# Kernel optimization log

Hardware: AMD Instinct MI355X
Metric: run time of the kernel (lower is better)

The kernel has to match this reference:

```python
import jax, jax.numpy as jnp
import numpy as np

N = 50000      # nodes
E = 800000     # edges (before self loops)
IN = 128       # in_channels
C = 64         # out_channels per head
H = 4          # heads (both layers)
NEG_SLOPE = 0.2


def setup_inputs():
    key = jax.random.key(0)
    ks = jax.random.split(key, 14)
    nrm = lambda k, sh, s: jax.random.normal(k, sh, dtype=jnp.float32) * s
    x = nrm(ks[0], (N, IN), 1.0)
    edge_index = jax.random.randint(ks[1], (2, E), 0, N, dtype=jnp.int32)
    batch = jnp.zeros((N,), dtype=jnp.int32)
    edge_attr = jax.random.uniform(ks[2], (E, 1), dtype=jnp.float32)
    # layer 1 params (PyG GATConv: lin, att_src, att_dst, lin_edge, att_edge, bias)
    W1 = nrm(ks[3], (IN, H * C), 1.0 / np.sqrt(IN))
    We1 = nrm(ks[4], (1, H * C), 1.0)
    att_s1 = nrm(ks[5], (H, C), 1.0 / np.sqrt(C))
    att_d1 = nrm(ks[6], (H, C), 1.0 / np.sqrt(C))
    att_e1 = nrm(ks[7], (H, C), 1.0 / np.sqrt(C))
    b1 = jnp.zeros((H * C,), dtype=jnp.float32)
    # layer 2 params (in = H*C = 256)
    W2 = nrm(ks[8], (H * C, H * C), 1.0 / np.sqrt(H * C))
    We2 = nrm(ks[9], (1, H * C), 1.0)
    att_s2 = nrm(ks[10], (H, C), 1.0 / np.sqrt(C))
    att_d2 = nrm(ks[11], (H, C), 1.0 / np.sqrt(C))
    att_e2 = nrm(ks[12], (H, C), 1.0 / np.sqrt(C))
    b2 = jnp.zeros((H * C,), dtype=jnp.float32)
    return dict(x=x, edge_index=edge_index, batch=batch, edge_attr=edge_attr,
                W1=W1, We1=We1, att_s1=att_s1, att_d1=att_d1, att_e1=att_e1, b1=b1,
                W2=W2, We2=We2, att_s2=att_s2, att_d2=att_d2, att_e2=att_e2, b2=b2)


def gat_layer(h_in, src, dst, e_attr, W, We, att_s, att_d, att_e, b):
    n = h_in.shape[0]
    h = (h_in @ W).reshape(n, H, C)                      # [N,H,C]
    a_src = jnp.einsum('nhc,hc->nh', h, att_s)           # [N,H]
    a_dst = jnp.einsum('nhc,hc->nh', h, att_d)
    e = (e_attr @ We).reshape(-1, H, C)                  # [E',H,C]
    a_edge = jnp.einsum('ehc,hc->eh', e, att_e)          # [E',H]
    alpha = jax.nn.leaky_relu(a_src[src] + a_dst[dst] + a_edge, NEG_SLOPE)
    # softmax over edges grouped by destination node
    amax = jax.ops.segment_max(alpha, dst, num_segments=n)
    amax = jnp.where(jnp.isfinite(amax), amax, 0.0)
    ex = jnp.exp(alpha - amax[dst])
    denom = jax.ops.segment_sum(ex, dst, num_segments=n)
    a = ex / (denom[dst] + 1e-16)                        # [E',H]
    out = jax.ops.segment_sum(a[:, :, None] * h[src], dst, num_segments=n)
    return out.reshape(n, H * C) + b


def reference(x, edge_index, batch, edge_attr,
              W1, We1, att_s1, att_d1, att_e1, b1,
              W2, We2, att_s2, att_d2, att_e2, b2):
    n = x.shape[0]
    # PyG GATConv default: add self loops, self-loop edge_attr = mean fill
    loop = jnp.arange(n, dtype=edge_index.dtype)
    src = jnp.concatenate([edge_index[0], loop])
    dst = jnp.concatenate([edge_index[1], loop])
    ea_fill = jnp.broadcast_to(edge_attr.mean(axis=0, keepdims=True), (n, edge_attr.shape[1]))
    ea = jnp.concatenate([edge_attr, ea_fill], axis=0)
    h1 = gat_layer(x, src, dst, ea, W1, We1, att_s1, att_d1, att_e1, b1)
    h2 = gat_layer(h1, src, dst, ea, W2, We2, att_s2, att_d2, att_e2, b2)
    return h2
```

## Files before the change

### kernel.cpp

```cpp
#include <hip/hip_runtime.h>

#define NEG_SLOPE 0.2f

typedef __attribute__((ext_vector_type(8))) short bf16x8;
typedef __attribute__((ext_vector_type(4))) float f32x4;

__device__ inline unsigned short f2bf(float x) {
  unsigned int u = __float_as_uint(x);
  u += 0x7fffu + ((u >> 16) & 1u);
  return (unsigned short)(u >> 16);
}

__device__ inline unsigned fkey(float x) {
  unsigned u = __float_as_uint(x);
  return (u >> 31) ? ~u : (u | 0x80000000u);
}
__device__ inline float fkey_dec(unsigned k) {
  unsigned u = (k & 0x80000000u) ? (k ^ 0x80000000u) : ~k;
  return __uint_as_float(u);
}


__global__ void hist_kernel(const int* __restrict__ ei, int* __restrict__ counts,
                            int E, int Etot) {
  int e = blockIdx.x * blockDim.x + threadIdx.x;
  if (e >= Etot) return;
  int d = (e < E) ? ei[E + e] : (e - E);
  atomicAdd(&counts[d], 1);
}

__global__ void mean_kernel(const float* __restrict__ ea, float* __restrict__ part, int E) {
  int i = blockIdx.x * blockDim.x + threadIdx.x;
  float s = 0.f;
  for (; i < E; i += gridDim.x * blockDim.x) s += ea[i];
#pragma unroll
  for (int off = 1; off < 64; off <<= 1) s += __shfl_xor(s, off, 64);
  __shared__ float ws_[4];
  if ((threadIdx.x & 63) == 0) ws_[threadIdx.x >> 6] = s;
  __syncthreads();
  if (threadIdx.x == 0) part[blockIdx.x] = ws_[0] + ws_[1] + ws_[2] + ws_[3];
}

__global__ void scan_blocksum(const int* __restrict__ counts, int* __restrict__ bsum, int Nn) {
  int base = blockIdx.x * 4096 + threadIdx.x * 16;
  int s = 0;
#pragma unroll
  for (int i = 0; i < 16; i++) { int idx = base + i; if (idx < Nn) s += counts[idx]; }
#pragma unroll
  for (int off = 1; off < 64; off <<= 1) s += __shfl_xor(s, off, 64);
  __shared__ int ws_[4];
  if ((threadIdx.x & 63) == 0) ws_[threadIdx.x >> 6] = s;
  __syncthreads();
  if (threadIdx.x == 0) bsum[blockIdx.x] = ws_[0] + ws_[1] + ws_[2] + ws_[3];
}

__global__ void scan_offsets(int* bsum, int nb, int* rowptrN,
                             const float* __restrict__ meanpart, float* meanv,
                             int E, int npart) {
  int t = threadIdx.x;
  float f = 0.f;
  for (int i = t; i < npart; i += 64) f += meanpart[i];
#pragma unroll
  for (int off = 1; off < 64; off <<= 1) f += __shfl_xor(f, off, 64);
  if (t == 0) {
    *meanv = f / (float)E;
    int acc = 0;
    for (int i = 0; i < nb; i++) { int v = bsum[i]; bsum[i] = acc; acc += v; }
    *rowptrN = acc;
  }
}

__global__ void scan_final(const int* __restrict__ counts, const int* __restrict__ bsum,
                           int* __restrict__ rowptr, int* __restrict__ cursor, int Nn) {
  int base = blockIdx.x * 4096 + threadIdx.x * 16;
  int v[16]; int s = 0;
#pragma unroll
  for (int i = 0; i < 16; i++) { int idx = base + i; v[i] = (idx < Nn) ? counts[idx] : 0; s += v[i]; }
  int lane = threadIdx.x & 63, wv = threadIdx.x >> 6;
  int incl = s;
#pragma unroll
  for (int off = 1; off < 64; off <<= 1) {
    int y = __shfl_up(incl, off, 64);
    if (lane >= off) incl += y;
  }
  __shared__ int wtot[4];
  if (lane == 63) wtot[wv] = incl;
  __syncthreads();
  int run = bsum[blockIdx.x] + incl - s;
  for (int i = 0; i < wv; i++) run += wtot[i];
  for (int i = 0; i < 16; i++) {
    int idx = base + i;
    if (idx < Nn) { rowptr[idx] = run; cursor[idx] = run; }
    run += v[i];
  }
}

__global__ void scatter_kernel(const int* __restrict__ ei, const float* __restrict__ eattr,
                               const float* __restrict__ meanv,
                               int* __restrict__ cursor, int2* __restrict__ epack,
                               int E, int Etot) {
  int e = blockIdx.x * blockDim.x + threadIdx.x;
  if (e >= Etot) return;
  int d, s; float ea;
  if (e < E) { d = ei[E + e]; s = ei[e]; ea = eattr[e]; }
  else       { d = e - E;     s = e - E; ea = meanv[0]; }
  int pos = atomicAdd(&cursor[d], 1);
  epack[pos] = make_int2(s, __float_as_int(ea));
}

__global__ void wtrans_kernel(const float* __restrict__ W1, unsigned short* __restrict__ Wt1,
                              const float* __restrict__ W2, unsigned short* __restrict__ Wt2,
                              const float* __restrict__ We1, const float* __restrict__ atte1,
                              const float* __restrict__ We2, const float* __restrict__ atte2,
                              float* __restrict__ weatt1, float* __restrict__ weatt2) {
  int b = blockIdx.x;
  if (b >= 384) {
    int i = threadIdx.x;
#pragma unroll
    for (int l = 0; l < 2; l++) {
      const float* We = l ? We2 : We1;
      const float* at = l ? atte2 : atte1;
      float* wo = l ? weatt2 : weatt1;
      float p = We[i] * at[i];
#pragma unroll
      for (int off = 1; off < 64; off <<= 1) p += __shfl_xor(p, off, 64);
      if ((i & 63) == 0) wo[i >> 6] = p;
    }
    return;
  }
  const float* W; unsigned short* Wt; int K, t;
  if (b < 128) { W = W1; Wt = Wt1; K = 128; t = b * 256 + threadIdx.x; }
  else         { W = W2; Wt = Wt2; K = 256; t = (b - 128) * 256 + threadIdx.x; }
  int n = t & 255, k = t >> 8;
  if (k >= K) return;
  Wt[(size_t)n * K + k] = f2bf(W[(size_t)k * 256 + n]);
}


template <int AF32>
__device__ inline bf16x8 load_a_row(const void* Ain, int gr, int K, int kpos, int M) {
  bf16x8 v = {};
  if (gr < M) {
    if (AF32) {
      const float* src = (const float*)Ain + (size_t)gr * K + kpos;
      float4 f0 = *(const float4*)src;
      float4 f1 = *(const float4*)(src + 4);
      v[0] = (short)f2bf(f0.x); v[1] = (short)f2bf(f0.y);
      v[2] = (short)f2bf(f0.z); v[3] = (short)f2bf(f0.w);
      v[4] = (short)f2bf(f1.x); v[5] = (short)f2bf(f1.y);
      v[6] = (short)f2bf(f1.z); v[7] = (short)f2bf(f1.w);
    } else {
      v = *(const bf16x8*)((const unsigned short*)Ain + (size_t)gr * K + kpos);
    }
  }
  return v;
}

#define CS_STRIDE 264

template <int AF32>
__global__ __launch_bounds__(512) void gemm_att(const void* __restrict__ Ain,
                                                const unsigned short* __restrict__ Wt,
                                                unsigned short* __restrict__ Hb,
                                                const float* __restrict__ atts,
                                                const float* __restrict__ attd,
                                                float* __restrict__ asrc,
                                                float* __restrict__ adst,
                                                unsigned* __restrict__ gmaxk,
                                                int M, int K) {
  __shared__ __align__(16) short smem[(128 + 256) * 64];
  __shared__ float gmx[8];
  short* As = smem;
  short* Bs = smem + 128 * 64;
  short* Cs = smem;
  const int tid = threadIdx.x;
  const int lane = tid & 63, wv = tid >> 6;
  const int wm = wv >> 2, wn = wv & 3;
  const int l15 = lane & 15, l4 = lane >> 4;
  const int bm = blockIdx.x * 128;

  const int r0 = tid >> 3, kc = (tid & 7) * 8;
  const int nbB = tid >> 3, cB = (tid & 7) * 8;

  f32x4 acc[4][4] = {};
  bf16x8 ra0, ra1, rb0, rb1, rb2, rb3;

#define GLOAD_TILE(K0, A0, A1, B0, B1, B2, B3)                                 \
  {                                                                            \
    A0 = load_a_row<AF32>(Ain, bm + r0, K, (K0) + kc, M);                      \
    A1 = load_a_row<AF32>(Ain, bm + r0 + 64, K, (K0) + kc, M);                 \
    B0 = *(const bf16x8*)&Wt[(size_t)(nbB +   0) * K + (K0) + cB];             \
    B1 = *(const bf16x8*)&Wt[(size_t)(nbB +  64) * K + (K0) + cB];             \
    B2 = *(const bf16x8*)&Wt[(size_t)(nbB + 128) * K + (K0) + cB];             \
    B3 = *(const bf16x8*)&Wt[(size_t)(nbB + 192) * K + (K0) + cB];             \
  }

  GLOAD_TILE(0, ra0, ra1, rb0, rb1, rb2, rb3)

  for (int k0 = 0; k0 < K; k0 += 64) {
    *(bf16x8*)&As[((r0) * 64 + kc) ^ ((r0 & 7) << 3)] = ra0;
    *(bf16x8*)&As[((r0 + 64) * 64 + kc) ^ ((r0 & 7) << 3)] = ra1;
    *(bf16x8*)&Bs[((nbB) * 64 + cB) ^ ((nbB & 7) << 3)] = rb0;
    *(bf16x8*)&Bs[((nbB + 64) * 64 + cB) ^ ((nbB & 7) << 3)] = rb1;
    *(bf16x8*)&Bs[((nbB + 128) * 64 + cB) ^ ((nbB & 7) << 3)] = rb2;
    *(bf16x8*)&Bs[((nbB + 192) * 64 + cB) ^ ((nbB & 7) << 3)] = rb3;
    __syncthreads();

    bool more = (k0 + 64 < K);
    bf16x8 na0, na1, nb0, nb1, nb2, nb3;
    if (more) GLOAD_TILE(k0 + 64, na0, na1, nb0, nb1, nb2, nb3)

    bf16x8 af[4][2], bfr[4][2];
#pragma unroll
    for (int rt = 0; rt < 4; rt++)
#pragma unroll
      for (int ks = 0; ks < 2; ks++) {
        int row = wm * 64 + rt * 16 + l15;
        int kb = l4 * 8 + ks * 32;
        af[rt][ks] = *(const bf16x8*)&As[(row * 64 + kb) ^ ((row & 7) << 3)];
      }
#pragma unroll
    for (int ct = 0; ct < 4; ct++)
#pragma unroll
      for (int ks = 0; ks < 2; ks++) {
        int n = wn * 64 + ct * 16 + l15;
        int kb = l4 * 8 + ks * 32;
        bfr[ct][ks] = *(const bf16x8*)&Bs[(n * 64 + kb) ^ ((n & 7) << 3)];
      }
#pragma unroll
    for (int rt = 0; rt < 4; rt++)
#pragma unroll
      for (int ct = 0; ct < 4; ct++)
#pragma unroll
        for (int ks = 0; ks < 2; ks++)
          acc[rt][ct] = __builtin_amdgcn_mfma_f32_16x16x32_bf16(
              af[rt][ks], bfr[ct][ks], acc[rt][ct], 0, 0, 0);
    __syncthreads();

    if (more) { ra0 = na0; ra1 = na1; rb0 = nb0; rb1 = nb1; rb2 = nb2; rb3 = nb3; }
  }
#undef GLOAD_TILE

  float s_att[4], d_att[4];
#pragma unroll
  for (int ct = 0; ct < 4; ct++) {
    s_att[ct] = atts[wn * 64 + ct * 16 + l15];
    d_att[ct] = attd[wn * 64 + ct * 16 + l15];
  }
  float ps[4][4] = {}, pd[4][4] = {};
#pragma unroll
  for (int rt = 0; rt < 4; rt++)
#pragma unroll
    for (int ct = 0; ct < 4; ct++)
#pragma unroll
      for (int i = 0; i < 4; i++) {
        float v = acc[rt][ct][i];
        ps[rt][i] = fmaf(v, s_att[ct], ps[rt][i]);
        pd[rt][i] = fmaf(v, d_att[ct], pd[rt][i]);
      }

#pragma unroll
  for (int rt = 0; rt < 4; rt++)
#pragma unroll
    for (int i = 0; i < 4; i++) {
#pragma unroll
      for (int off = 1; off < 16; off <<= 1) {
        ps[rt][i] += __shfl_xor(ps[rt][i], off, 64);
        pd[rt][i] += __shfl_xor(pd[rt][i], off, 64);
      }
    }
  float mx = ps[0][0];
#pragma unroll
  for (int rt = 0; rt < 4; rt++)
#pragma unroll
    for (int i = 0; i < 4; i++) mx = fmaxf(mx, ps[rt][i]);
  mx = fmaxf(mx, __shfl_xor(mx, 16, 64));
  mx = fmaxf(mx, __shfl_xor(mx, 32, 64));
  if (lane == 0) gmx[wv] = mx;
  if (l15 == 0) {
#pragma unroll
    for (int rt = 0; rt < 4; rt++)
#pragma unroll
      for (int i = 0; i < 4; i++) {
        int gr = bm + wm * 64 + rt * 16 + l4 * 4 + i;
        if (gr < M) {
          asrc[gr * 4 + wn] = ps[rt][i];
          adst[gr * 4 + wn] = pd[rt][i];
        }
      }
  }

  for (int h = 0; h < 2; h++) {
    __syncthreads();
    if (wm == h) {
#pragma unroll
      for (int rt = 0; rt < 4; rt++)
#pragma unroll
        for (int ct = 0; ct < 4; ct++)
#pragma unroll
          for (int i = 0; i < 4; i++) {
            int lrow = rt * 16 + l4 * 4 + i;
            Cs[lrow * CS_STRIDE + wn * 64 + ct * 16 + l15] = f2bf(acc[rt][ct][i]);
          }
    }
    __syncthreads();
    int row = tid >> 3, seg = tid & 7;
    int gr = bm + h * 64 + row;
    if (gr < M) {
      const short* srcr = &Cs[row * CS_STRIDE + seg * 32];
      unsigned short* dstr = &Hb[(size_t)gr * 256 + seg * 32];
#pragma unroll
      for (int k = 0; k < 4; k++)
        *(uint4*)&dstr[k * 8] = *(const uint4*)&srcr[k * 8];
    }
  }

  if (wv < 4 && lane == 0) {
    float m2 = fmaxf(gmx[wv], gmx[wv + 4]);
    atomicMax(&gmaxk[wv * 32], fkey(m2));
  }
}


#define AGG_PH1(CNT)                                                        \
  int src = 0; float w = 0.f;                                               \
  if (il < (CNT)) {                                                         \
    int2 e = epack[p + il];                                                 \
    float al = fmaf(__int_as_float(e.y), wa, asrc[e.x * 4 + hh] + ad);      \
    al = fmaxf(al, NEG_SLOPE * al);                                         \
    w = __expf(al - b);                                                     \
    src = e.x;                                                              \
  }                                                                         \
  ssum += w;

#define AGG_GATHER(i)                                                       \
  {                                                                         \
    int sl = (i) | hb16;                                                    \
    int si = __shfl(src, sl, 64);                                           \
    float wi = __shfl(w, sl, 64);                                           \
    uint2 hv = *(const uint2*)&Hb[(size_t)((unsigned)si * 256u + co)];      \
    acc.x = fmaf(wi, __uint_as_float(hv.x << 16), acc.x);                   \
    acc.y = fmaf(wi, __uint_as_float(hv.x & 0xffff0000u), acc.y);           \
    acc.z = fmaf(wi, __uint_as_float(hv.y << 16), acc.z);                   \
    acc.w = fmaf(wi, __uint_as_float(hv.y & 0xffff0000u), acc.w);           \
  }

template <int OUTBF>
__global__ __launch_bounds__(256) void gat_agg(const unsigned short* __restrict__ Hb,
                                               const float* __restrict__ asrc,
                                               const float* __restrict__ adst,
                                               const int* __restrict__ rowptr,
                                               const int2* __restrict__ epack,
                                               const float* __restrict__ weatt,
                                               const unsigned* __restrict__ gmaxk,
                                               const float* __restrict__ bias,
                                               unsigned short* __restrict__ outb,
                                               float* __restrict__ outf, int Nn) {
  int wid = (blockIdx.x * blockDim.x + threadIdx.x) >> 6;
  int lane = threadIdx.x & 63;
  if (wid >= Nn) return;
  int beg = rowptr[wid], end = rowptr[wid + 1];
  int hh = lane >> 4;
  int il = lane & 15;
  int hb16 = lane & 48;
  float wa = weatt[hh];
  float ad = adst[wid * 4 + hh];
  float braw = ad + fkey_dec(gmaxk[hh * 32]) + fmaxf(wa, 0.f);
  float b = fmaxf(braw, NEG_SLOPE * braw);
  unsigned co = (unsigned)lane * 4u;

  float ssum = 0.f;
  float4 acc = {0.f, 0.f, 0.f, 0.f};

  int p = beg;
  for (; p + 16 <= end; p += 16) {
    AGG_PH1(16)
#pragma unroll
    for (int i = 0; i < 16; i++) AGG_GATHER(i)
  }
  int cnt = end - p;
  if (cnt > 0) {
    AGG_PH1(cnt)
    for (int i = 0; i < cnt; i++) AGG_GATHER(i)
  }

#pragma unroll
  for (int off = 1; off < 16; off <<= 1) ssum += __shfl_xor(ssum, off, 64);

  float inv = 1.f / (ssum + 1e-16f);
  float4 b4 = *(const float4*)&bias[co];
  float4 r;
  r.x = fmaf(acc.x, inv, b4.x);
  r.y = fmaf(acc.y, inv, b4.y);
  r.z = fmaf(acc.z, inv, b4.z);
  r.w = fmaf(acc.w, inv, b4.w);
  if (OUTBF) {
    unsigned lo = (unsigned)f2bf(r.x) | ((unsigned)f2bf(r.y) << 16);
    unsigned hi = (unsigned)f2bf(r.z) | ((unsigned)f2bf(r.w) << 16);
    *(uint2*)&outb[(size_t)wid * 256 + co] = make_uint2(lo, hi);
  } else {
    *(float4*)&outf[(size_t)wid * 256 + co] = r;
  }
}


extern "C" void kernel_launch(void* const* d_in, const int* in_sizes, int n_in,
                              void* d_out, int out_size, void* d_ws, size_t ws_size,
                              hipStream_t stream) {
  (void)n_in; (void)out_size; (void)ws_size;
  const float* x     = (const float*)d_in[0];
  const int*   ei    = (const int*)d_in[1];
  const float* eattr = (const float*)d_in[3];
  const float* W1    = (const float*)d_in[4];
  const float* We1   = (const float*)d_in[5];
  const float* atts1 = (const float*)d_in[6];
  const float* attd1 = (const float*)d_in[7];
  const float* atte1 = (const float*)d_in[8];
  const float* b1    = (const float*)d_in[9];
  const float* W2    = (const float*)d_in[10];
  const float* We2   = (const float*)d_in[11];
  const float* atts2 = (const float*)d_in[12];
  const float* attd2 = (const float*)d_in[13];
  const float* atte2 = (const float*)d_in[14];
  const float* b2    = (const float*)d_in[15];
  float* out = (float*)d_out;

  const int Nn   = in_sizes[0] / 128;
  const int E    = in_sizes[1] / 2;
  const int Etot = E + Nn;

  char* p = (char*)d_ws;
  auto alloc = [&](size_t bytes) { void* r = (void*)p; p += (bytes + 255) & ~(size_t)255; return r; };
  int*      counts  = (int*)alloc((size_t)Nn * 4);
  unsigned* gmaxk1  = (unsigned*)alloc(512);
  unsigned* gmaxk2  = (unsigned*)alloc(512);
  char* zero_end = p;
  int*   rowptr  = (int*)alloc((size_t)(Nn + 1) * 4);
  int*   cursor  = (int*)alloc((size_t)Nn * 4);
  int2*  epack   = (int2*)alloc((size_t)Etot * 8);
  int*   bsum    = (int*)alloc(64 * 4);
  float* meanpart= (float*)alloc(512 * 4);
  float* meanv   = (float*)alloc(4);
  float* weatt1  = (float*)alloc(16);
  float* weatt2  = (float*)alloc(16);
  float* asrc    = (float*)alloc((size_t)Nn * 4 * 4);
  float* adst    = (float*)alloc((size_t)Nn * 4 * 4);
  unsigned short* hbuf = (unsigned short*)alloc((size_t)Nn * 256 * 2);
  unsigned short* h1b  = (unsigned short*)alloc((size_t)Nn * 256 * 2);
  unsigned short* Wt1  = (unsigned short*)alloc((size_t)256 * 128 * 2);
  unsigned short* Wt2  = (unsigned short*)alloc((size_t)256 * 256 * 2);

  const int NB = (Nn + 4095) / 4096;

  hipMemsetAsync(counts, 0, (size_t)(zero_end - (char*)counts), stream);

  hist_kernel<<<(Etot + 255) / 256, 256, 0, stream>>>(ei, counts, E, Etot);
  mean_kernel<<<512, 256, 0, stream>>>(eattr, meanpart, E);
  scan_blocksum<<<NB, 256, 0, stream>>>(counts, bsum, Nn);
  scan_offsets<<<1, 64, 0, stream>>>(bsum, NB, rowptr + Nn, meanpart, meanv, E, 512);
  scan_final<<<NB, 256, 0, stream>>>(counts, bsum, rowptr, cursor, Nn);
  scatter_kernel<<<(Etot + 255) / 256, 256, 0, stream>>>(ei, eattr, meanv, cursor, epack, E, Etot);
  wtrans_kernel<<<385, 256, 0, stream>>>(W1, Wt1, W2, Wt2, We1, atte1, We2, atte2,
                                         weatt1, weatt2);

  const int gemmBlocks = (Nn + 127) / 128;
  const int nodeBlocks = (Nn + 3) / 4;

  gemm_att<1><<<gemmBlocks, 512, 0, stream>>>(x, Wt1, hbuf, atts1, attd1,
                                              asrc, adst, gmaxk1, Nn, 128);
  gat_agg<1><<<nodeBlocks, 256, 0, stream>>>(hbuf, asrc, adst, rowptr, epack,
                                             weatt1, gmaxk1, b1, h1b, nullptr, Nn);
  gemm_att<0><<<gemmBlocks, 512, 0, stream>>>(h1b, Wt2, hbuf, atts2, attd2,
                                              asrc, adst, gmaxk2, Nn, 256);
  gat_agg<0><<<nodeBlocks, 256, 0, stream>>>(hbuf, asrc, adst, rowptr, epack,
                                             weatt2, gmaxk2, b2, nullptr, out, Nn);
}
```

Measured before the change: 320.1 us.

## Shrink GEMM tile to 64 rows with 4 waves and drop register prefetch

The fused GEMM+attention kernel now uses 64-row tiles with 256 threads, where each wave owns one head's 64 columns. The register double-buffered global prefetch is removed, and tiles are loaded straight into LDS each iteration. The bf16 epilogue store happens in one pass, and per-wave atomicMax replaces the LDS-staged block reduction. The aim is more blocks and lower LDS per block for better occupancy and a simpler epilogue. The cost is twice as many W tile loads per output row, no overlap of global loads with MFMA, and twice as many atomics.

```diff
diff --git a/kernel.cpp b/kernel.cpp
--- a/kernel.cpp
+++ b/kernel.cpp
@@ -159,7 +159,7 @@
 #define CS_STRIDE 264
 
 template <int AF32>
-__global__ __launch_bounds__(512) void gemm_att(const void* __restrict__ Ain,
+__global__ __launch_bounds__(256) void gemm_att(const void* __restrict__ Ain,
                                                 const unsigned short* __restrict__ Wt,
                                                 unsigned short* __restrict__ Hb,
                                                 const float* __restrict__ atts,
@@ -168,54 +168,41 @@
                                                 float* __restrict__ adst,
                                                 unsigned* __restrict__ gmaxk,
                                                 int M, int K) {
-  __shared__ __align__(16) short smem[(128 + 256) * 64];
-  __shared__ float gmx[8];
+  __shared__ __align__(16) short smem[(64 + 256) * 64];
   short* As = smem;
-  short* Bs = smem + 128 * 64;
+  short* Bs = smem + 64 * 64;
   short* Cs = smem;
   const int tid = threadIdx.x;
   const int lane = tid & 63, wv = tid >> 6;
-  const int wm = wv >> 2, wn = wv & 3;
   const int l15 = lane & 15, l4 = lane >> 4;
-  const int bm = blockIdx.x * 128;
-
-  const int r0 = tid >> 3, kc = (tid & 7) * 8;
-  const int nbB = tid >> 3, cB = (tid & 7) * 8;
+  const int bm = blockIdx.x * 64;
 
   f32x4 acc[4][4] = {};
-  bf16x8 ra0, ra1, rb0, rb1, rb2, rb3;
-
-#define GLOAD_TILE(K0, A0, A1, B0, B1, B2, B3)                                 \
-  {                                                                            \
-    A0 = load_a_row<AF32>(Ain, bm + r0, K, (K0) + kc, M);                      \
-    A1 = load_a_row<AF32>(Ain, bm + r0 + 64, K, (K0) + kc, M);                 \
-    B0 = *(const bf16x8*)&Wt[(size_t)(nbB +   0) * K + (K0) + cB];             \
-    B1 = *(const bf16x8*)&Wt[(size_t)(nbB +  64) * K + (K0) + cB];             \
-    B2 = *(const bf16x8*)&Wt[(size_t)(nbB + 128) * K + (K0) + cB];             \
-    B3 = *(const bf16x8*)&Wt[(size_t)(nbB + 192) * K + (K0) + cB];             \
-  }
-
-  GLOAD_TILE(0, ra0, ra1, rb0, rb1, rb2, rb3)
 
   for (int k0 = 0; k0 < K; k0 += 64) {
-    *(bf16x8*)&As[((r0) * 64 + kc) ^ ((r0 & 7) << 3)] = ra0;
-    *(bf16x8*)&As[((r0 + 64) * 64 + kc) ^ ((r0 & 7) << 3)] = ra1;
-    *(bf16x8*)&Bs[((nbB) * 64 + cB) ^ ((nbB & 7) << 3)] = rb0;
-    *(bf16x8*)&Bs[((nbB + 64) * 64 + cB) ^ ((nbB & 7) << 3)] = rb1;
-    *(bf16x8*)&Bs[((nbB + 128) * 64 + cB) ^ ((nbB & 7) << 3)] = rb2;
-    *(bf16x8*)&Bs[((nbB + 192) * 64 + cB) ^ ((nbB & 7) << 3)] = rb3;
+    {
+      int r0 = tid >> 3, kcc = (tid & 7) * 8;
+      bf16x8 va0 = load_a_row<AF32>(Ain, bm + r0, K, k0 + kcc, M);
+      bf16x8 va1 = load_a_row<AF32>(Ain, bm + r0 + 32, K, k0 + kcc, M);
+      *(bf16x8*)&As[(r0 * 64 + kcc) ^ ((r0 & 7) << 3)] = va0;
+      *(bf16x8*)&As[((r0 + 32) * 64 + kcc) ^ ((r0 & 7) << 3)] = va1;
+    }
+    {
+      int nb = tid >> 3, c = (tid & 7) * 8;
+#pragma unroll
+      for (int it = 0; it < 8; it++) {
+        int n = nb + 32 * it;
+        bf16x8 v = *(const bf16x8*)&Wt[(size_t)n * K + k0 + c];
+        *(bf16x8*)&Bs[(n * 64 + c) ^ ((n & 7) << 3)] = v;
+      }
+    }
     __syncthreads();
-
-    bool more = (k0 + 64 < K);
-    bf16x8 na0, na1, nb0, nb1, nb2, nb3;
-    if (more) GLOAD_TILE(k0 + 64, na0, na1, nb0, nb1, nb2, nb3)
-
     bf16x8 af[4][2], bfr[4][2];
 #pragma unroll
     for (int rt = 0; rt < 4; rt++)
 #pragma unroll
       for (int ks = 0; ks < 2; ks++) {
-        int row = wm * 64 + rt * 16 + l15;
+        int row = rt * 16 + l15;
         int kb = l4 * 8 + ks * 32;
         af[rt][ks] = *(const bf16x8*)&As[(row * 64 + kb) ^ ((row & 7) << 3)];
       }
@@ -223,7 +210,7 @@
     for (int ct = 0; ct < 4; ct++)
 #pragma unroll
       for (int ks = 0; ks < 2; ks++) {
-        int n = wn * 64 + ct * 16 + l15;
+        int n = wv * 64 + ct * 16 + l15;
         int kb = l4 * 8 + ks * 32;
         bfr[ct][ks] = *(const bf16x8*)&Bs[(n * 64 + kb) ^ ((n & 7) << 3)];
       }
@@ -236,16 +223,13 @@
           acc[rt][ct] = __builtin_amdgcn_mfma_f32_16x16x32_bf16(
               af[rt][ks], bfr[ct][ks], acc[rt][ct], 0, 0, 0);
     __syncthreads();
-
-    if (more) { ra0 = na0; ra1 = na1; rb0 = nb0; rb1 = nb1; rb2 = nb2; rb3 = nb3; }
-  }
-#undef GLOAD_TILE
+  }
 
   float s_att[4], d_att[4];
 #pragma unroll
   for (int ct = 0; ct < 4; ct++) {
-    s_att[ct] = atts[wn * 64 + ct * 16 + l15];
-    d_att[ct] = attd[wn * 64 + ct * 16 + l15];
+    s_att[ct] = atts[wv * 64 + ct * 16 + l15];
+    d_att[ct] = attd[wv * 64 + ct * 16 + l15];
   }
   float ps[4][4] = {}, pd[4][4] = {};
 #pragma unroll
@@ -255,9 +239,24 @@
 #pragma unroll
       for (int i = 0; i < 4; i++) {
         float v = acc[rt][ct][i];
+        int lrow = rt * 16 + l4 * 4 + i;
+        Cs[lrow * CS_STRIDE + wv * 64 + ct * 16 + l15] = f2bf(v);
         ps[rt][i] = fmaf(v, s_att[ct], ps[rt][i]);
         pd[rt][i] = fmaf(v, d_att[ct], pd[rt][i]);
       }
+  __syncthreads();
+
+  {
+    int row = tid >> 2, seg = tid & 3;
+    int gr = bm + row;
+    if (gr < M) {
+      const short* srcr = &Cs[row * CS_STRIDE + seg * 64];
+      unsigned short* dstr = &Hb[(size_t)gr * 256 + seg * 64];
+#pragma unroll
+      for (int k = 0; k < 8; k++)
+        *(uint4*)&dstr[k * 8] = *(const uint4*)&srcr[k * 8];
+    }
+  }
 
 #pragma unroll
   for (int rt = 0; rt < 4; rt++)
@@ -276,48 +275,18 @@
     for (int i = 0; i < 4; i++) mx = fmaxf(mx, ps[rt][i]);
   mx = fmaxf(mx, __shfl_xor(mx, 16, 64));
   mx = fmaxf(mx, __shfl_xor(mx, 32, 64));
-  if (lane == 0) gmx[wv] = mx;
+  if (lane == 0) atomicMax(&gmaxk[wv * 32], fkey(mx));
   if (l15 == 0) {
 #pragma unroll
     for (int rt = 0; rt < 4; rt++)
 #pragma unroll
       for (int i = 0; i < 4; i++) {
-        int gr = bm + wm * 64 + rt * 16 + l4 * 4 + i;
+        int gr = bm + rt * 16 + l4 * 4 + i;
         if (gr < M) {
-          asrc[gr * 4 + wn] = ps[rt][i];
-          adst[gr * 4 + wn] = pd[rt][i];
+          asrc[gr * 4 + wv] = ps[rt][i];
+          adst[gr * 4 + wv] = pd[rt][i];
         }
       }
-  }
-
-  for (int h = 0; h < 2; h++) {
-    __syncthreads();
-    if (wm == h) {
-#pragma unroll
-      for (int rt = 0; rt < 4; rt++)
-#pragma unroll
-        for (int ct = 0; ct < 4; ct++)
-#pragma unroll
-          for (int i = 0; i < 4; i++) {
-            int lrow = rt * 16 + l4 * 4 + i;
-            Cs[lrow * CS_STRIDE + wn * 64 + ct * 16 + l15] = f2bf(acc[rt][ct][i]);
-          }
-    }
-    __syncthreads();
-    int row = tid >> 3, seg = tid & 7;
-    int gr = bm + h * 64 + row;
-    if (gr < M) {
-      const short* srcr = &Cs[row * CS_STRIDE + seg * 32];
-      unsigned short* dstr = &Hb[(size_t)gr * 256 + seg * 32];
-#pragma unroll
-      for (int k = 0; k < 4; k++)
-        *(uint4*)&dstr[k * 8] = *(const uint4*)&srcr[k * 8];
-    }
-  }
-
-  if (wv < 4 && lane == 0) {
-    float m2 = fmaxf(gmx[wv], gmx[wv + 4]);
-    atomicMax(&gmaxk[wv * 32], fkey(m2));
   }
 }
 
@@ -463,14 +432,14 @@
   wtrans_kernel<<<385, 256, 0, stream>>>(W1, Wt1, W2, Wt2, We1, atte1, We2, atte2,
                                          weatt1, weatt2);
 
-  const int gemmBlocks = (Nn + 127) / 128;
+  const int gemmBlocks = (Nn + 63) / 64;
   const int nodeBlocks = (Nn + 3) / 4;
 
-  gemm_att<1><<<gemmBlocks, 512, 0, stream>>>(x, Wt1, hbuf, atts1, attd1,
+  gemm_att<1><<<gemmBlocks, 256, 0, stream>>>(x, Wt1, hbuf, atts1, attd1,
                                               asrc, adst, gmaxk1, Nn, 128);
   gat_agg<1><<<nodeBlocks, 256, 0, stream>>>(hbuf, asrc, adst, rowptr, epack,
                                              weatt1, gmaxk1, b1, h1b, nullptr, Nn);
-  gemm_att<0><<<gemmBlocks, 512, 0, stream>>>(h1b, Wt2, hbuf, atts2, attd2,
+  gemm_att<0><<<gemmBlocks, 256, 0, stream>>>(h1b, Wt2, hbuf, atts2, attd2,
                                               asrc, adst, gmaxk2, Nn, 256);
   gat_agg<0><<<nodeBlocks, 256, 0, stream>>>(hbuf, asrc, adst, rowptr, epack,
                                              weatt2, gmaxk2, b2, nullptr, out, Nn);
```

New measurement: 330.3 us. +3.2%, slower.

## Replace global-atomic edge scatter with per-block destination-partitioned LDS scatter

Applied to the files above, without the earlier changes.

Removes the cursor array and the global atomic scatter. Each of 256 blocks now owns a contiguous range of destination nodes, scans the whole destination index list, and places its edges with shared-memory atomics. Self loops are appended last per node. This avoids global atomic contention and gives localized writes, but every block reads the full edge list, which multiplies memory traffic, and one block per CU limits parallelism.

```diff
diff --git a/kernel.cpp b/kernel.cpp
--- a/kernel.cpp
+++ b/kernel.cpp
@@ -71,7 +71,7 @@
 }
 
 __global__ void scan_final(const int* __restrict__ counts, const int* __restrict__ bsum,
-                           int* __restrict__ rowptr, int* __restrict__ cursor, int Nn) {
+                           int* __restrict__ rowptr, int Nn) {
   int base = blockIdx.x * 4096 + threadIdx.x * 16;
   int v[16]; int s = 0;
 #pragma unroll
@@ -90,22 +90,53 @@
   for (int i = 0; i < wv; i++) run += wtot[i];
   for (int i = 0; i < 16; i++) {
     int idx = base + i;
-    if (idx < Nn) { rowptr[idx] = run; cursor[idx] = run; }
+    if (idx < Nn) rowptr[idx] = run;
     run += v[i];
   }
 }
 
-__global__ void scatter_kernel(const int* __restrict__ ei, const float* __restrict__ eattr,
-                               const float* __restrict__ meanv,
-                               int* __restrict__ cursor, int2* __restrict__ epack,
-                               int E, int Etot) {
-  int e = blockIdx.x * blockDim.x + threadIdx.x;
-  if (e >= Etot) return;
-  int d, s; float ea;
-  if (e < E) { d = ei[E + e]; s = ei[e]; ea = eattr[e]; }
-  else       { d = e - E;     s = e - E; ea = meanv[0]; }
-  int pos = atomicAdd(&cursor[d], 1);
-  epack[pos] = make_int2(s, __float_as_int(ea));
+
+__global__ __launch_bounds__(256) void scatter_part(const int* __restrict__ ei,
+                                                    const float* __restrict__ eattr,
+                                                    const float* __restrict__ meanv,
+                                                    const int* __restrict__ rowptr,
+                                                    int2* __restrict__ epack,
+                                                    int E, int Nn, int dpb) {
+  __shared__ int cur[256];
+  int d0 = blockIdx.x * dpb;
+  int d1 = d0 + dpb; if (d1 > Nn) d1 = Nn;
+  int nd = d1 - d0;
+  for (int i = threadIdx.x; i < nd; i += 256) cur[i] = rowptr[d0 + i];
+  __syncthreads();
+  if (nd <= 0) return;
+  const int t = threadIdx.x;
+  const int* dstp = ei + E;
+  int e4 = E >> 2;
+  for (int g = t; g < e4; g += 256) {
+    int4 dv = ((const int4*)dstp)[g];
+    int ebase = g * 4;
+#pragma unroll
+    for (int j = 0; j < 4; j++) {
+      int d = (&dv.x)[j];
+      if (d >= d0 && d < d1) {
+        int e = ebase + j;
+        int pos = atomicAdd(&cur[d - d0], 1);
+        epack[pos] = make_int2(ei[e], __float_as_int(eattr[e]));
+      }
+    }
+  }
+  for (int e = (e4 << 2) + t; e < E; e += 256) {
+    int d = dstp[e];
+    if (d >= d0 && d < d1) {
+      int pos = atomicAdd(&cur[d - d0], 1);
+      epack[pos] = make_int2(ei[e], __float_as_int(eattr[e]));
+    }
+  }
+  float mea = meanv[0];
+  for (int d = d0 + t; d < d1; d += 256) {
+    int pos = atomicAdd(&cur[d - d0], 1);
+    epack[pos] = make_int2(d, __float_as_int(mea));
+  }
 }
 
 __global__ void wtrans_kernel(const float* __restrict__ W1, unsigned short* __restrict__ Wt1,
@@ -436,7 +467,6 @@
   unsigned* gmaxk2  = (unsigned*)alloc(512);
   char* zero_end = p;
   int*   rowptr  = (int*)alloc((size_t)(Nn + 1) * 4);
-  int*   cursor  = (int*)alloc((size_t)Nn * 4);
   int2*  epack   = (int2*)alloc((size_t)Etot * 8);
   int*   bsum    = (int*)alloc(64 * 4);
   float* meanpart= (float*)alloc(512 * 4);
@@ -451,6 +481,8 @@
   unsigned short* Wt2  = (unsigned short*)alloc((size_t)256 * 256 * 2);
 
   const int NB = (Nn + 4095) / 4096;
+  const int SCB = 256;
+  const int dpb = (Nn + SCB - 1) / SCB;
 
   hipMemsetAsync(counts, 0, (size_t)(zero_end - (char*)counts), stream);
 
@@ -458,8 +490,8 @@
   mean_kernel<<<512, 256, 0, stream>>>(eattr, meanpart, E);
   scan_blocksum<<<NB, 256, 0, stream>>>(counts, bsum, Nn);
   scan_offsets<<<1, 64, 0, stream>>>(bsum, NB, rowptr + Nn, meanpart, meanv, E, 512);
-  scan_final<<<NB, 256, 0, stream>>>(counts, bsum, rowptr, cursor, Nn);
-  scatter_kernel<<<(Etot + 255) / 256, 256, 0, stream>>>(ei, eattr, meanv, cursor, epack, E, Etot);
+  scan_final<<<NB, 256, 0, stream>>>(counts, bsum, rowptr, Nn);
+  scatter_part<<<SCB, 256, 0, stream>>>(ei, eattr, meanv, rowptr, epack, E, Nn, dpb);
   wtrans_kernel<<<385, 256, 0, stream>>>(W1, Wt1, W2, Wt2, We1, atte1, We2, atte2,
                                          weatt1, weatt2);
 
```

Result: slower. 608.4 us (+90.1%).
